# Optimization experiments

Hardware: AMD Instinct MI355X
Metric: run time of the kernel (lower is better)

Reference implementation:

```python
import jax, jax.numpy as jnp
import numpy as np

N_NODES = 50000


def gcn_conv(x, W, src, dst, n):
    # PyG GCNConv(bias=False): h = x @ W, then symmetric-normalized
    # aggregation over A + I (self-loops added, normalize=True).
    h = x @ W  # [N, F_out]
    loop = jnp.arange(n, dtype=src.dtype)
    s = jnp.concatenate([src, loop])  # source nodes (messages come from x_j = h[s])
    d = jnp.concatenate([dst, loop])  # target nodes (aggregation index)
    ones = jnp.ones(s.shape[0], dtype=h.dtype)
    deg = jax.ops.segment_sum(ones, d, num_segments=n)  # in-degree incl. self-loop
    dinv = jnp.where(deg > 0, jax.lax.rsqrt(deg), 0.0)
    norm = dinv[s] * dinv[d]  # per-edge D^-1/2 A_hat D^-1/2 weight
    msgs = h[s] * norm[:, None]  # gather + scale
    return jax.ops.segment_sum(msgs, d, num_segments=n)  # scatter-add


def setup_inputs() -> dict:
    key = jax.random.key(0)
    k1, k2, k3, k4 = jax.random.split(key, 4)
    x = jax.random.normal(k1, (N_NODES, 256), dtype=jnp.float32)
    edge_index = jax.random.randint(k2, (2, 1600000), 0, N_NODES, dtype=jnp.int64)
    # glorot-scale weights
    W1 = jax.random.normal(k3, (256, 256), dtype=jnp.float32) * (1.0 / np.sqrt(256))
    W3 = jax.random.normal(k4, (256, 64), dtype=jnp.float32) * (1.0 / np.sqrt(256))
    return {"x": x, "edge_index": edge_index, "W1": W1, "W3": W3}


def reference(x, edge_index, W1, W3):
    n = x.shape[0]
    src, dst = edge_index[0], edge_index[1]
    h = jax.nn.relu(gcn_conv(x, W1, src, dst, n))
    h = jax.nn.relu(gcn_conv(h, W3, src, dst, n))
    return h
```

## Files before the change

kernel.cpp:

```cpp
#include <hip/hip_runtime.h>
#include <cstdint>
#include <cstddef>


#define NPART 128

__device__ __forceinline__ float bf2f(unsigned short u) {
    union { unsigned int i; float f; } c; c.i = ((unsigned int)u) << 16; return c.f;
}
__device__ __forceinline__ unsigned short f2bf(float f) {
    union { float f; unsigned int i; } c; c.f = f;
    unsigned int r = c.i + 0x7fffu + ((c.i >> 16) & 1u);
    return (unsigned short)(r >> 16);
}

__global__ __launch_bounds__(256) void wcvt2_kernel(const float* __restrict__ W1,
                                                    const float* __restrict__ W3,
                                                    unsigned short* __restrict__ W1t,
                                                    unsigned short* __restrict__ W3t) {
    int idx = blockIdx.x * 256 + threadIdx.x;
    if (idx < 256 * 256) {
        int nn = idx >> 8, kk = idx & 255;
        W1t[idx] = f2bf(W1[kk * 256 + nn]);
    } else if (idx < 256 * 256 + 64 * 256) {
        int j = idx - 256 * 256;
        int nn = j >> 8, kk = j & 255;
        W3t[j] = f2bf(W3[kk * 64 + nn]);
    }
}


__global__ __launch_bounds__(256) void part_hist(const int* __restrict__ dst, int E, int NB,
                                                 int* __restrict__ blockhist) {
    __shared__ int lh[1024];
    for (int t = threadIdx.x; t < NB; t += 256) lh[t] = 0;
    __syncthreads();
    const int per = (E + NPART - 1) / NPART;
    const int beg = blockIdx.x * per;
    const int end = min(E, beg + per);
    for (int i = beg + threadIdx.x; i < end; i += 256)
        atomicAdd(&lh[dst[i] >> 6], 1);
    __syncthreads();
    for (int t = threadIdx.x; t < NB; t += 256)
        blockhist[blockIdx.x * NB + t] = lh[t];
}

__global__ __launch_bounds__(1024) void part_scan(const int* __restrict__ blockhist,
                                                  int* __restrict__ bofs,
                                                  int* __restrict__ bbase, int NB) {
    __shared__ int wsum[16];
    const int t = threadIdx.x;
    const int lane = t & 63;
    int tot = 0;
    if (t < NB) {
        #pragma unroll 4
        for (int k = 0; k < NPART; ++k) tot += blockhist[k * NB + t];
    }
    int x = tot;
    #pragma unroll
    for (int off = 1; off < 64; off <<= 1) {
        int q = __shfl_up(x, off);
        if (lane >= off) x += q;
    }
    if (lane == 63) wsum[t >> 6] = x;
    __syncthreads();
    if (t < 64) {
        int y = (t < 16) ? wsum[t] : 0;
        #pragma unroll
        for (int off = 1; off < 16; off <<= 1) {
            int q = __shfl_up(y, off);
            if (lane >= off) y += q;
        }
        if (t < 16) wsum[t] = y;
    }
    __syncthreads();
    int excl = ((t >> 6) ? wsum[(t >> 6) - 1] : 0) + x - tot;
    if (t < NB) {
        bofs[t] = excl;
        if (t == NB - 1) bofs[NB] = excl + tot;
        int run = excl;
        for (int k = 0; k < NPART; ++k) {
            int c = blockhist[k * NB + t];
            bbase[k * NB + t] = run;
            run += c;
        }
    }
}

__global__ __launch_bounds__(256) void part_scatter(const int* __restrict__ src,
                                                    const int* __restrict__ dst,
                                                    const int* __restrict__ bbase,
                                                    unsigned int* __restrict__ words,
                                                    int E, int NB) {
    __shared__ int lbase[1024];
    for (int t = threadIdx.x; t < NB; t += 256) lbase[t] = bbase[blockIdx.x * NB + t];
    __syncthreads();
    const int per = (E + NPART - 1) / NPART;
    const int beg = blockIdx.x * per;
    const int end = min(E, beg + per);
    for (int i = beg + threadIdx.x; i < end; i += 256) {
        int d = dst[i];
        int off = atomicAdd(&lbase[d >> 6], 1);
        words[off] = ((unsigned)src[i] << 6) | (unsigned)(d & 63);
    }
}

__global__ __launch_bounds__(256) void bucket_build(const unsigned int* __restrict__ words,
                                                    const int* __restrict__ bofs,
                                                    int* __restrict__ rowptr,
                                                    float* __restrict__ dinv,
                                                    int* __restrict__ csr, int n) {
    const int b = blockIdx.x;
    const int node0 = b << 6;
    __shared__ int ldeg[64], lcur[64];
    if (threadIdx.x < 64) ldeg[threadIdx.x] = 0;
    __syncthreads();
    const int beg = bofs[b], end = bofs[b + 1];
    for (int i = beg + threadIdx.x; i < end; i += 256)
        atomicAdd(&ldeg[words[i] & 63u], 1);
    __syncthreads();
    if (threadIdx.x < 64) {
        const int lane = threadIdx.x;
        int v = ldeg[lane];
        int x = v;
        #pragma unroll
        for (int off = 1; off < 64; off <<= 1) {
            int q = __shfl_up(x, off);
            if (lane >= off) x += q;
        }
        int excl = x - v;
        int node = node0 + lane;
        if (node < n) {
            rowptr[node] = beg + excl;
            dinv[node] = rsqrtf((float)(v + 1));
        }
        lcur[lane] = beg + excl;
        if (b == (int)gridDim.x - 1 && lane == 0) rowptr[n] = end;
    }
    __syncthreads();
    for (int i = beg + threadIdx.x; i < end; i += 256) {
        unsigned int w = words[i];
        int pos = atomicAdd(&lcur[w & 63u], 1);
        csr[pos] = (int)(w >> 6);
    }
}

template<int BN, int WM, int WN, bool AF32>
__global__ __launch_bounds__(256) void mfma_gemm(const void* __restrict__ Av,
                                                 const unsigned short* __restrict__ Bt,
                                                 const float* __restrict__ dinvp,
                                                 unsigned short* __restrict__ C,
                                                 int M, int N, int K) {
    constexpr int BM = 128, BK = 64;
    constexpr int KP = 72;
    constexpr int WTM = BM / WM;
    constexpr int WTN = BN / WN;
    constexpr int MF = WTM / 16;
    constexpr int NF = WTN / 16;
    __shared__ unsigned short As[BM][KP];
    __shared__ unsigned short Bs[BN][KP];
    const int tid = threadIdx.x;
    const int wid = tid >> 6;
    const int lane = tid & 63;
    const int wr = wid / WN;
    const int wc = wid % WN;
    const int bm = blockIdx.y * BM;
    const int bn = blockIdx.x * BN;
    const int l15 = lane & 15;
    const int lg = lane >> 4;

    using bf16x8 = __attribute__((ext_vector_type(8))) short;
    using f32x4  = __attribute__((ext_vector_type(4))) float;
    f32x4 acc[MF][NF] = {};

    for (int k0 = 0; k0 < K; k0 += BK) {
        #pragma unroll
        for (int it = 0; it < (BM * BK / 8) / 256; ++it) {
            int v = tid + 256 * it;
            int row = v >> 3;
            int oct = v & 7;
            uint4 val = make_uint4(0, 0, 0, 0);
            int gr = bm + row;
            if (gr < M) {
                if (AF32) {
                    const float* A32 = (const float*)Av;
                    float4 f0 = *(const float4*)(A32 + (size_t)gr * K + k0 + oct * 8);
                    float4 f1 = *(const float4*)(A32 + (size_t)gr * K + k0 + oct * 8 + 4);
                    union { unsigned short u[8]; uint4 v4; } pk;
                    pk.u[0] = f2bf(f0.x); pk.u[1] = f2bf(f0.y);
                    pk.u[2] = f2bf(f0.z); pk.u[3] = f2bf(f0.w);
                    pk.u[4] = f2bf(f1.x); pk.u[5] = f2bf(f1.y);
                    pk.u[6] = f2bf(f1.z); pk.u[7] = f2bf(f1.w);
                    val = pk.v4;
                } else {
                    const unsigned short* Ab = (const unsigned short*)Av;
                    val = *(const uint4*)(Ab + (size_t)gr * K + k0 + oct * 8);
                }
            }
            *(uint4*)(&As[row][oct * 8]) = val;
        }
        #pragma unroll
        for (int it = 0; it < (BN * BK / 8) / 256; ++it) {
            int v = tid + 256 * it;
            int row = v >> 3;
            int oct = v & 7;
            uint4 val = *(const uint4*)(Bt + (size_t)(bn + row) * K + k0 + oct * 8);
            *(uint4*)(&Bs[row][oct * 8]) = val;
        }
        __syncthreads();
        #pragma unroll
        for (int kk = 0; kk < 2; ++kk) {
            bf16x8 af[MF], bfr[NF];
            #pragma unroll
            for (int m = 0; m < MF; ++m)
                af[m] = *(const bf16x8*)(&As[wr * WTM + m * 16 + l15][kk * 32 + lg * 8]);
            #pragma unroll
            for (int nf = 0; nf < NF; ++nf)
                bfr[nf] = *(const bf16x8*)(&Bs[wc * WTN + nf * 16 + l15][kk * 32 + lg * 8]);
            #pragma unroll
            for (int m = 0; m < MF; ++m)
                #pragma unroll
                for (int nf = 0; nf < NF; ++nf)
                    acc[m][nf] = __builtin_amdgcn_mfma_f32_16x16x32_bf16(
                        af[m], bfr[nf], acc[m][nf], 0, 0, 0);
        }
        __syncthreads();
    }
    #pragma unroll
    for (int m = 0; m < MF; ++m) {
        #pragma unroll
        for (int j = 0; j < 4; ++j) {
            int row = bm + wr * WTM + m * 16 + lg * 4 + j;
            if (row < M) {
                float s = dinvp[row];
                #pragma unroll
                for (int nf = 0; nf < NF; ++nf) {
                    int col = bn + wc * WTN + nf * 16 + l15;
                    C[(size_t)row * N + col] = f2bf(acc[m][nf][j] * s);
                }
            }
        }
    }
}

__global__ __launch_bounds__(256) void aggregate256_kernel(
        const unsigned short* __restrict__ hs, const int* __restrict__ rowptr,
        const int* __restrict__ csr, const float* __restrict__ dinv,
        unsigned short* __restrict__ out, int n) {
    const int d = blockIdx.x;
    const int tid = threadIdx.x;
    const int wid = tid >> 6;
    const int lane = tid & 63;
    const int beg = rowptr[d];
    const int end = rowptr[d + 1];

    float acc0 = 0.f, acc1 = 0.f, acc2 = 0.f, acc3 = 0.f;
    if (wid == 0) {
        ushort4 t = *(const ushort4*)(hs + (size_t)d * 256 + lane * 4);
        acc0 = bf2f(t.x); acc1 = bf2f(t.y); acc2 = bf2f(t.z); acc3 = bf2f(t.w);
    }

    __shared__ unsigned int soff[256];
    const char* hb = (const char*)hs;
    for (int k0 = beg; k0 < end; k0 += 256) {
        int cnt = min(256, end - k0);
        if (tid < cnt) soff[tid] = (unsigned)csr[k0 + tid] * 512u;
        __syncthreads();
        #pragma unroll 8
        for (int e = wid; e < cnt; e += 4) {
            ushort4 t = *(const ushort4*)(hb + soff[e] + lane * 8);
            acc0 += bf2f(t.x); acc1 += bf2f(t.y);
            acc2 += bf2f(t.z); acc3 += bf2f(t.w);
        }
        __syncthreads();
    }

    __shared__ float part[3][256];
    if (wid > 0) {
        part[wid - 1][lane * 4 + 0] = acc0;
        part[wid - 1][lane * 4 + 1] = acc1;
        part[wid - 1][lane * 4 + 2] = acc2;
        part[wid - 1][lane * 4 + 3] = acc3;
    }
    __syncthreads();
    if (wid == 0) {
        const float wd = dinv[d];
        acc0 += part[0][lane*4+0] + part[1][lane*4+0] + part[2][lane*4+0];
        acc1 += part[0][lane*4+1] + part[1][lane*4+1] + part[2][lane*4+1];
        acc2 += part[0][lane*4+2] + part[1][lane*4+2] + part[2][lane*4+2];
        acc3 += part[0][lane*4+3] + part[1][lane*4+3] + part[2][lane*4+3];
        union { unsigned short u[4]; uint2 v; } pk;
        pk.u[0] = f2bf(fmaxf(wd * acc0, 0.f));
        pk.u[1] = f2bf(fmaxf(wd * acc1, 0.f));
        pk.u[2] = f2bf(fmaxf(wd * acc2, 0.f));
        pk.u[3] = f2bf(fmaxf(wd * acc3, 0.f));
        *(uint2*)(out + (size_t)d * 256 + lane * 4) = pk.v;
    }
}

__global__ __launch_bounds__(256) void aggregate64_kernel(
        const unsigned short* __restrict__ hs, const int* __restrict__ rowptr,
        const int* __restrict__ csr, const float* __restrict__ dinv,
        float* __restrict__ out, int n) {
    const int d = blockIdx.x;
    const int tid = threadIdx.x;
    const int wid = tid >> 6;
    const int lane = tid & 63;
    const int beg = rowptr[d];
    const int end = rowptr[d + 1];

    float acc = 0.f;
    if (wid == 0) acc = bf2f(hs[(size_t)d * 64 + lane]);

    __shared__ unsigned int soff[256];
    const char* hb = (const char*)hs;
    for (int k0 = beg; k0 < end; k0 += 256) {
        int cnt = min(256, end - k0);
        if (tid < cnt) soff[tid] = (unsigned)csr[k0 + tid] * 128u;
        __syncthreads();
        #pragma unroll 8
        for (int e = wid; e < cnt; e += 4) {
            unsigned short t = *(const unsigned short*)(hb + soff[e] + lane * 2);
            acc += bf2f(t);
        }
        __syncthreads();
    }

    __shared__ float part[3][64];
    if (wid > 0) part[wid - 1][lane] = acc;
    __syncthreads();
    if (wid == 0) {
        acc += part[0][lane] + part[1][lane] + part[2][lane];
        out[(size_t)d * 64 + lane] = fmaxf(dinv[d] * acc, 0.f);
    }
}


static inline size_t align256(size_t v) { return (v + 255) & ~(size_t)255; }

extern "C" void kernel_launch(void* const* d_in, const int* in_sizes, int n_in,
                              void* d_out, int out_size, void* d_ws, size_t ws_size,
                              hipStream_t stream) {
    const float* x  = (const float*)d_in[0];
    const int*   ei = (const int*)d_in[1];
    const float* W1 = (const float*)d_in[2];
    const float* W3 = (const float*)d_in[3];

    const int n = in_sizes[0] / 256;
    const int E = in_sizes[1] / 2;
    const int NB = (n + 63) >> 6;
    const int* src = ei;
    const int* dst = ei + E;

    char* w = (char*)d_ws;
    auto alloc = [&](size_t bytes) { char* p = w; w += align256(bytes); return p; };
    unsigned short* hs1  = (unsigned short*)alloc((size_t)n * 256 * 2);
    unsigned short* a1   = (unsigned short*)alloc((size_t)n * 256 * 2);
    unsigned short* hs2  = (unsigned short*)alloc((size_t)n * 64 * 2);
    unsigned short* W1t  = (unsigned short*)alloc(256 * 256 * 2);
    unsigned short* W3t  = (unsigned short*)alloc(64 * 256 * 2);
    float* dinv          = (float*)alloc((size_t)n * 4);
    int*   rowptr        = (int*)alloc((size_t)(n + 1) * 4);
    int*   csr           = (int*)alloc((size_t)E * 4);
    unsigned int* words  = (unsigned int*)alloc((size_t)E * 4);
    int*   blockhist     = (int*)alloc((size_t)NPART * NB * 4);
    int*   bbase         = (int*)alloc((size_t)NPART * NB * 4);
    int*   bofs          = (int*)alloc((size_t)(NB + 1) * 4);
    float* out           = (float*)d_out;

    wcvt2_kernel<<<(256 * 256 + 64 * 256 + 255) / 256, 256, 0, stream>>>(W1, W3, W1t, W3t);

    part_hist<<<NPART, 256, 0, stream>>>(dst, E, NB, blockhist);
    part_scan<<<1, 1024, 0, stream>>>(blockhist, bofs, bbase, NB);
    part_scatter<<<NPART, 256, 0, stream>>>(src, dst, bbase, words, E, NB);
    bucket_build<<<NB, 256, 0, stream>>>(words, bofs, rowptr, dinv, csr, n);

    {
        dim3 grid(1, (n + 127) / 128);
        mfma_gemm<256, 2, 2, true><<<grid, 256, 0, stream>>>(x, W1t, dinv, hs1, n, 256, 256);
        aggregate256_kernel<<<n, 256, 0, stream>>>(hs1, rowptr, csr, dinv, a1, n);
    }
    {
        dim3 grid(1, (n + 127) / 128);
        mfma_gemm<64, 4, 1, false><<<grid, 256, 0, stream>>>(a1, W3t, dinv, hs2, n, 64, 256);
        aggregate64_kernel<<<n, 256, 0, stream>>>(hs2, rowptr, csr, dinv, out, n);
    }
}
```

Measured before the change: 309.0 us.

## Store first GEMM output in 32-column slices and aggregate per slice

The first-layer GEMM writes its bf16 output as eight feature slices of 32 columns each (slice-major), and a new aggregation kernel gathers neighbour rows within one slice, one half-wave per destination node. This is meant to shrink the gathered working set so random neighbour reads hit in cache, and to remove the shared-memory staging and cross-wave reduction. It trades this for narrow 2-byte per-lane loads, strided output writes, and load imbalance across nodes of different degree.

```diff
diff --git a/kernel.cpp b/kernel.cpp
--- a/kernel.cpp
+++ b/kernel.cpp
@@ -145,7 +145,7 @@
     }
 }
 
-template<int BN, int WM, int WN, bool AF32>
+template<int BN, int WM, int WN, bool AF32, bool CTILED>
 __global__ __launch_bounds__(256) void mfma_gemm(const void* __restrict__ Av,
                                                  const unsigned short* __restrict__ Bt,
                                                  const float* __restrict__ dinvp,
@@ -236,66 +236,50 @@
                 #pragma unroll
                 for (int nf = 0; nf < NF; ++nf) {
                     int col = bn + wc * WTN + nf * 16 + l15;
-                    C[(size_t)row * N + col] = f2bf(acc[m][nf][j] * s);
+                    unsigned short v = f2bf(acc[m][nf][j] * s);
+                    if (CTILED)
+                        C[((size_t)(col >> 5) * M + row) * 32 + (col & 31)] = v;
+                    else
+                        C[(size_t)row * N + col] = v;
                 }
             }
         }
     }
 }
 
-__global__ __launch_bounds__(256) void aggregate256_kernel(
-        const unsigned short* __restrict__ hs, const int* __restrict__ rowptr,
+__global__ __launch_bounds__(256) void agg256_tiled(
+        const unsigned short* __restrict__ hst, const int* __restrict__ rowptr,
         const int* __restrict__ csr, const float* __restrict__ dinv,
         unsigned short* __restrict__ out, int n) {
-    const int d = blockIdx.x;
-    const int tid = threadIdx.x;
-    const int wid = tid >> 6;
-    const int lane = tid & 63;
+    const int t = blockIdx.x & 7;
+    const int g = blockIdx.x >> 3;
+    const int wv = threadIdx.x >> 6;
+    const int half = (threadIdx.x >> 5) & 1;
+    const int c = threadIdx.x & 31;
+    const int d = g * 8 + wv * 2 + half;
+    if (d >= n) return;
+    const unsigned short* slice = hst + (size_t)t * n * 32;
+
+    float acc = bf2f(slice[(size_t)d * 32 + c]);
     const int beg = rowptr[d];
-    const int end = rowptr[d + 1];
-
-    float acc0 = 0.f, acc1 = 0.f, acc2 = 0.f, acc3 = 0.f;
-    if (wid == 0) {
-        ushort4 t = *(const ushort4*)(hs + (size_t)d * 256 + lane * 4);
-        acc0 = bf2f(t.x); acc1 = bf2f(t.y); acc2 = bf2f(t.z); acc3 = bf2f(t.w);
-    }
-
-    __shared__ unsigned int soff[256];
-    const char* hb = (const char*)hs;
-    for (int k0 = beg; k0 < end; k0 += 256) {
-        int cnt = min(256, end - k0);
-        if (tid < cnt) soff[tid] = (unsigned)csr[k0 + tid] * 512u;
-        __syncthreads();
-        #pragma unroll 8
-        for (int e = wid; e < cnt; e += 4) {
-            ushort4 t = *(const ushort4*)(hb + soff[e] + lane * 8);
-            acc0 += bf2f(t.x); acc1 += bf2f(t.y);
-            acc2 += bf2f(t.z); acc3 += bf2f(t.w);
-        }
-        __syncthreads();
-    }
-
-    __shared__ float part[3][256];
-    if (wid > 0) {
-        part[wid - 1][lane * 4 + 0] = acc0;
-        part[wid - 1][lane * 4 + 1] = acc1;
-        part[wid - 1][lane * 4 + 2] = acc2;
-        part[wid - 1][lane * 4 + 3] = acc3;
-    }
-    __syncthreads();
-    if (wid == 0) {
-        const float wd = dinv[d];
-        acc0 += part[0][lane*4+0] + part[1][lane*4+0] + part[2][lane*4+0];
-        acc1 += part[0][lane*4+1] + part[1][lane*4+1] + part[2][lane*4+1];
-        acc2 += part[0][lane*4+2] + part[1][lane*4+2] + part[2][lane*4+2];
-        acc3 += part[0][lane*4+3] + part[1][lane*4+3] + part[2][lane*4+3];
-        union { unsigned short u[4]; uint2 v; } pk;
-        pk.u[0] = f2bf(fmaxf(wd * acc0, 0.f));
-        pk.u[1] = f2bf(fmaxf(wd * acc1, 0.f));
-        pk.u[2] = f2bf(fmaxf(wd * acc2, 0.f));
-        pk.u[3] = f2bf(fmaxf(wd * acc3, 0.f));
-        *(uint2*)(out + (size_t)d * 256 + lane * 4) = pk.v;
-    }
+    const int deg = rowptr[d + 1] - beg;
+
+    int k = 0;
+    for (; k + 4 <= deg; k += 4) {
+        int s0 = csr[beg + k];
+        int s1 = csr[beg + k + 1];
+        int s2 = csr[beg + k + 2];
+        int s3 = csr[beg + k + 3];
+        float v0 = bf2f(slice[(size_t)s0 * 32 + c]);
+        float v1 = bf2f(slice[(size_t)s1 * 32 + c]);
+        float v2 = bf2f(slice[(size_t)s2 * 32 + c]);
+        float v3 = bf2f(slice[(size_t)s3 * 32 + c]);
+        acc += (v0 + v1) + (v2 + v3);
+    }
+    for (; k < deg; ++k)
+        acc += bf2f(slice[(size_t)csr[beg + k] * 32 + c]);
+
+    out[(size_t)d * 256 + t * 32 + c] = f2bf(fmaxf(dinv[d] * acc, 0.f));
 }
 
 __global__ __launch_bounds__(256) void aggregate64_kernel(
@@ -354,7 +338,7 @@
 
     char* w = (char*)d_ws;
     auto alloc = [&](size_t bytes) { char* p = w; w += align256(bytes); return p; };
-    unsigned short* hs1  = (unsigned short*)alloc((size_t)n * 256 * 2);
+    unsigned short* hs1t = (unsigned short*)alloc((size_t)n * 256 * 2);
     unsigned short* a1   = (unsigned short*)alloc((size_t)n * 256 * 2);
     unsigned short* hs2  = (unsigned short*)alloc((size_t)n * 64 * 2);
     unsigned short* W1t  = (unsigned short*)alloc(256 * 256 * 2);
@@ -377,12 +361,13 @@
 
     {
         dim3 grid(1, (n + 127) / 128);
-        mfma_gemm<256, 2, 2, true><<<grid, 256, 0, stream>>>(x, W1t, dinv, hs1, n, 256, 256);
-        aggregate256_kernel<<<n, 256, 0, stream>>>(hs1, rowptr, csr, dinv, a1, n);
+        mfma_gemm<256, 2, 2, true, true><<<grid, 256, 0, stream>>>(x, W1t, dinv, hs1t, n, 256, 256);
+        int ngrp = (n + 7) / 8;
+        agg256_tiled<<<ngrp * 8, 256, 0, stream>>>(hs1t, rowptr, csr, dinv, a1, n);
     }
     {
         dim3 grid(1, (n + 127) / 128);
-        mfma_gemm<64, 4, 1, false><<<grid, 256, 0, stream>>>(a1, W3t, dinv, hs2, n, 64, 256);
+        mfma_gemm<64, 4, 1, false, false><<<grid, 256, 0, stream>>>(a1, W3t, dinv, hs2, n, 64, 256);
         aggregate64_kernel<<<n, 256, 0, stream>>>(hs2, rowptr, csr, dinv, out, n);
     }
 }
```

New measurement: 369.9 us. +19.7%, slower.
